# Kernel optimization log

Measured on AMD Instinct MI355X. Metric: run time of the kernel, lower is better.

Reference implementation:

```python
import jax, jax.numpy as jnp
import numpy as np

BN_EPS = 1e-5
SAMPLE_KEY = jax.random.key(42)


def setup_inputs() -> dict:
    key = jax.random.key(0)
    ks = jax.random.split(key, 12)
    B, W, E = 524288, 8, 4
    D = W * E  # 32, input dim of fc1

    def lin(k, fan_in, fan_out):
        k1, k2 = jax.random.split(k)
        bound = 1.0 / np.sqrt(fan_in)
        w = jax.random.uniform(k1, (fan_in, fan_out), jnp.float32, -bound, bound)
        b = jax.random.uniform(k2, (fan_out,), jnp.float32, -bound, bound)
        return w, b

    W1, b1 = lin(ks[0], D, 50)
    W2, b2 = lin(ks[1], 50, 30)
    W3, b3 = lin(ks[2], 30, 20)
    W4, b4 = lin(ks[3], 20, 15)
    W5, b5 = lin(ks[4], 15, W)
    # BatchNorm affine params (eval mode, running_mean=0, running_var=1)
    g1, be1 = jnp.ones((50,), jnp.float32), jnp.zeros((50,), jnp.float32)
    g2, be2 = jnp.ones((30,), jnp.float32), jnp.zeros((30,), jnp.float32)
    g3, be3 = jnp.ones((20,), jnp.float32), jnp.zeros((20,), jnp.float32)
    events = jax.random.normal(ks[5], (B, W, E), jnp.float32)
    return {"events": events,
            "W1": W1, "b1": b1, "g1": g1, "be1": be1,
            "W2": W2, "b2": b2, "g2": g2, "be2": be2,
            "W3": W3, "b3": b3, "g3": g3, "be3": be3,
            "W4": W4, "b4": b4, "W5": W5, "b5": b5}


def _bn_eval(x, g, b):
    # eval-mode BatchNorm1d with running_mean=0, running_var=1
    return x * (g / jnp.sqrt(1.0 + BN_EPS)) + b


def _probs(events, W1, b1, g1, be1, W2, b2, g2, be2, W3, b3, g3, be3, W4, b4, W5, b5):
    B = events.shape[0]
    x = events.reshape(B, -1)  # (B, window*event_size)
    h = jax.nn.relu(_bn_eval(x @ W1 + b1, g1, be1))
    h = jax.nn.relu(_bn_eval(h @ W2 + b2, g2, be2))
    h = jax.nn.relu(_bn_eval(h @ W3 + b3, g3, be3))
    h = jax.nn.relu(h @ W4 + b4)
    return jax.nn.sigmoid(h @ W5 + b5)  # (B, window_size)


def reference(events, W1, b1, g1, be1, W2, b2, g2, be2, W3, b3, g3, be3, W4, b4, W5, b5):
    p = _probs(events, W1, b1, g1, be1, W2, b2, g2, be2, W3, b3, g3, be3, W4, b4, W5, b5)
    # np.random.choice([0,1], p=[p, 1-p]) => P(choice=1) = 1 - p
    choice = jax.random.bernoulli(SAMPLE_KEY, 1.0 - p).astype(p.dtype)  # (B, W)
    chosen_events_np = 1.0 - choice
    flipped = jnp.abs(choice - p)            # prob of sampled outcome per element
    log_prob = jnp.log(jnp.prod(flipped, axis=1))  # (B,)
    return chosen_events_np, log_prob
```

## Files before the change

### kernel.cpp

```cpp
#include <hip/hip_runtime.h>
#include <math.h>

#define THREADS 256
#define P_MARGIN 1e-4f
#define FIXCAP 32

typedef float v2f __attribute__((ext_vector_type(2)));

__device__ __forceinline__ void tf2x32(unsigned x0, unsigned x1,
                                       unsigned &o0, unsigned &o1) {
  const unsigned k0 = 0u;
  const unsigned k1 = 42u;
  const unsigned k2 = 0x1BD11BDAu ^ k0 ^ k1;
  x0 += k0; x1 += k1;
#define TF_R(r) { x0 += x1; x1 = (x1 << (r)) | (x1 >> (32 - (r))); x1 ^= x0; }
  TF_R(13) TF_R(15) TF_R(26) TF_R(6)
  x0 += k1; x1 += k2 + 1u;
  TF_R(17) TF_R(29) TF_R(16) TF_R(24)
  x0 += k2; x1 += k0 + 2u;
  TF_R(13) TF_R(15) TF_R(26) TF_R(6)
  x0 += k0; x1 += k1 + 3u;
  TF_R(17) TF_R(29) TF_R(16) TF_R(24)
  x0 += k1; x1 += k2 + 4u;
  TF_R(13) TF_R(15) TF_R(26) TF_R(6)
  x0 += k2; x1 += k0 + 5u;
#undef TF_R
  o0 = x0; o1 = x1;
}

__global__ __launch_bounds__(THREADS, 2)
void wtf_kernel(const float* __restrict__ events,
                const float* __restrict__ W1, const float* __restrict__ b1,
                const float* __restrict__ g1, const float* __restrict__ be1,
                const float* __restrict__ W2, const float* __restrict__ b2,
                const float* __restrict__ g2, const float* __restrict__ be2,
                const float* __restrict__ W3, const float* __restrict__ b3,
                const float* __restrict__ g3, const float* __restrict__ be3,
                const float* __restrict__ W4, const float* __restrict__ b4,
                const float* __restrict__ W5, const float* __restrict__ b5,
                float* __restrict__ out_chosen,
                float* __restrict__ out_logp,
                int B) {
  __shared__ unsigned s_cnt;
  __shared__ unsigned s_rows[FIXCAP];
  __shared__ double sA[64];
  __shared__ double sB[64];
  __shared__ double sF[8];

  const int t = threadIdx.x;
  if (t == 0) s_cnt = 0;
  __syncthreads();

  const int b = blockIdx.x * THREADS + t;
  const bool active = (b < B);
  const float rden = (float)(1.0 / sqrt(1.0 + 1e-5));

  if (active) {
    float x[32];
    const float4* ev4 = reinterpret_cast<const float4*>(events) + (size_t)b * 8;
#pragma unroll
    for (int q = 0; q < 8; ++q) {
      float4 v = ev4[q];
      x[4 * q + 0] = v.x; x[4 * q + 1] = v.y; x[4 * q + 2] = v.z; x[4 * q + 3] = v.w;
    }

    v2f A[25];
#pragma unroll
    for (int j = 0; j < 25; ++j) A[j] = v2f{b1[2 * j], b1[2 * j + 1]};
#pragma unroll
    for (int k = 0; k < 32; ++k) {
      const v2f xk2 = {x[k], x[k]};
#pragma unroll
      for (int j = 0; j < 25; ++j) {
        v2f w = {W1[k * 50 + 2 * j], W1[k * 50 + 2 * j + 1]};
        A[j] = __builtin_elementwise_fma(xk2, w, A[j]);
      }
    }
    float a1[50];
#pragma unroll
    for (int j = 0; j < 25; ++j) {
      a1[2 * j + 0] = fmaxf(fmaf(A[j].x, g1[2 * j + 0] * rden, be1[2 * j + 0]), 0.f);
      a1[2 * j + 1] = fmaxf(fmaf(A[j].y, g1[2 * j + 1] * rden, be1[2 * j + 1]), 0.f);
    }

    v2f C[15];
#pragma unroll
    for (int j = 0; j < 15; ++j) C[j] = v2f{b2[2 * j], b2[2 * j + 1]};
#pragma unroll
    for (int k = 0; k < 50; ++k) {
      const v2f hk2 = {a1[k], a1[k]};
#pragma unroll
      for (int j = 0; j < 15; ++j) {
        v2f w = {W2[k * 30 + 2 * j], W2[k * 30 + 2 * j + 1]};
        C[j] = __builtin_elementwise_fma(hk2, w, C[j]);
      }
    }
    float a2[30];
#pragma unroll
    for (int j = 0; j < 15; ++j) {
      a2[2 * j + 0] = fmaxf(fmaf(C[j].x, g2[2 * j + 0] * rden, be2[2 * j + 0]), 0.f);
      a2[2 * j + 1] = fmaxf(fmaf(C[j].y, g2[2 * j + 1] * rden, be2[2 * j + 1]), 0.f);
    }

    v2f D[10];
#pragma unroll
    for (int j = 0; j < 10; ++j) D[j] = v2f{b3[2 * j], b3[2 * j + 1]};
#pragma unroll
    for (int k = 0; k < 30; ++k) {
      const v2f hk2 = {a2[k], a2[k]};
#pragma unroll
      for (int j = 0; j < 10; ++j) {
        v2f w = {W3[k * 20 + 2 * j], W3[k * 20 + 2 * j + 1]};
        D[j] = __builtin_elementwise_fma(hk2, w, D[j]);
      }
    }
    float a3[20];
#pragma unroll
    for (int j = 0; j < 10; ++j) {
      a3[2 * j + 0] = fmaxf(fmaf(D[j].x, g3[2 * j + 0] * rden, be3[2 * j + 0]), 0.f);
      a3[2 * j + 1] = fmaxf(fmaf(D[j].y, g3[2 * j + 1] * rden, be3[2 * j + 1]), 0.f);
    }

    v2f E[7];
    float e14 = b4[14];
#pragma unroll
    for (int j = 0; j < 7; ++j) E[j] = v2f{b4[2 * j], b4[2 * j + 1]};
#pragma unroll
    for (int k = 0; k < 20; ++k) {
      const float hk = a3[k];
      const v2f hk2 = {hk, hk};
#pragma unroll
      for (int j = 0; j < 7; ++j) {
        v2f w = {W4[k * 15 + 2 * j], W4[k * 15 + 2 * j + 1]};
        E[j] = __builtin_elementwise_fma(hk2, w, E[j]);
      }
      e14 = fmaf(hk, W4[k * 15 + 14], e14);
    }
    float a4[15];
#pragma unroll
    for (int j = 0; j < 7; ++j) {
      a4[2 * j + 0] = fmaxf(E[j].x, 0.f);
      a4[2 * j + 1] = fmaxf(E[j].y, 0.f);
    }
    a4[14] = fmaxf(e14, 0.f);

    v2f P[4];
#pragma unroll
    for (int j = 0; j < 4; ++j) P[j] = v2f{b5[2 * j], b5[2 * j + 1]};
#pragma unroll
    for (int k = 0; k < 15; ++k) {
      const v2f hk2 = {a4[k], a4[k]};
#pragma unroll
      for (int j = 0; j < 4; ++j) {
        v2f w = {W5[k * 8 + 2 * j], W5[k * 8 + 2 * j + 1]};
        P[j] = __builtin_elementwise_fma(hk2, w, P[j]);
      }
    }
    float p[8];
#pragma unroll
    for (int j = 0; j < 4; ++j) {
      p[2 * j + 0] = 1.f / (1.f + expf(-P[j].x));
      p[2 * j + 1] = 1.f / (1.f + expf(-P[j].y));
    }

    bool need = false;
    float prod = 1.f;
    float ch[8];
#pragma unroll
    for (int w = 0; w < 8; ++w) {
      unsigned j = 8u * (unsigned)b + (unsigned)w, o0, o1;
      tf2x32(0u, j, o0, o1);
      unsigned bits = o0 ^ o1;
      float u = __uint_as_float(0x3F800000u | (bits >> 9)) - 1.f;
      float thr = 1.f - p[w];
      bool choice = u < thr;
      need = need || (fabsf(u - thr) < P_MARGIN);
      ch[w] = choice ? 0.f : 1.f;
      prod *= choice ? thr : p[w];
    }
    if (need) {
      unsigned i = atomicAdd(&s_cnt, 1u);
      if (i < FIXCAP) s_rows[i] = (unsigned)b;
    }

    float4* oc = reinterpret_cast<float4*>(out_chosen) + (size_t)b * 2;
    oc[0] = make_float4(ch[0], ch[1], ch[2], ch[3]);
    oc[1] = make_float4(ch[4], ch[5], ch[6], ch[7]);
    out_logp[b] = logf(prod);
  }

  __syncthreads();
  unsigned cnt = s_cnt;
  if (cnt > FIXCAP) cnt = FIXCAP;
  if (cnt == 0) return;

  const double denom = sqrt(1.0 + 1e-5);
  for (unsigned r = 0; r < cnt; ++r) {
    const int rb = (int)s_rows[r];

    if (t < 32) sA[t] = (double)events[(size_t)rb * 32 + t];
    __syncthreads();

    double v = 0.0;
    if (t < 50) {
#pragma unroll
      for (int k = 0; k < 32; ++k) v = fma(sA[k], (double)W1[k * 50 + t], v);
      v += (double)b1[t];
      v = v * ((double)g1[t] / denom) + (double)be1[t];
      v = v > 0.0 ? v : 0.0;
    }
    __syncthreads();
    if (t < 50) sB[t] = v;
    __syncthreads();

    v = 0.0;
    if (t < 30) {
#pragma unroll
      for (int k = 0; k < 50; ++k) v = fma(sB[k], (double)W2[k * 30 + t], v);
      v += (double)b2[t];
      v = v * ((double)g2[t] / denom) + (double)be2[t];
      v = v > 0.0 ? v : 0.0;
    }
    __syncthreads();
    if (t < 30) sA[t] = v;
    __syncthreads();

    v = 0.0;
    if (t < 20) {
#pragma unroll
      for (int k = 0; k < 30; ++k) v = fma(sA[k], (double)W3[k * 20 + t], v);
      v += (double)b3[t];
      v = v * ((double)g3[t] / denom) + (double)be3[t];
      v = v > 0.0 ? v : 0.0;
    }
    __syncthreads();
    if (t < 20) sB[t] = v;
    __syncthreads();

    v = 0.0;
    if (t < 15) {
#pragma unroll
      for (int k = 0; k < 20; ++k) v = fma(sB[k], (double)W4[k * 15 + t], v);
      v += (double)b4[t];
      v = v > 0.0 ? v : 0.0;
    }
    __syncthreads();
    if (t < 15) sA[t] = v;
    __syncthreads();

    if (t < 8) {
      v = 0.0;
#pragma unroll
      for (int k = 0; k < 15; ++k) v = fma(sA[k], (double)W5[k * 8 + t], v);
      v += (double)b5[t];
      double p = 1.0 / (1.0 + exp(-v));
      unsigned j = 8u * (unsigned)rb + (unsigned)t, o0, o1;
      tf2x32(0u, j, o0, o1);
      unsigned bits = o0 ^ o1;
      float u = __uint_as_float(0x3F800000u | (bits >> 9)) - 1.f;
      double thr = 1.0 - p;
      bool choice = ((double)u < thr);
      out_chosen[(size_t)rb * 8 + t] = choice ? 0.f : 1.f;
      sF[t] = choice ? thr : p;
    }
    __syncthreads();
    if (t == 0) {
      double prod = 1.0;
      for (int w = 0; w < 8; ++w) prod *= sF[w];
      out_logp[rb] = (float)log(prod);
    }
    __syncthreads();
  }
}

extern "C" void kernel_launch(void* const* d_in, const int* in_sizes, int n_in,
                              void* d_out, int out_size, void* d_ws, size_t ws_size,
                              hipStream_t stream) {
  const float* events = (const float*)d_in[0];
  const float* W1  = (const float*)d_in[1];
  const float* b1  = (const float*)d_in[2];
  const float* g1  = (const float*)d_in[3];
  const float* be1 = (const float*)d_in[4];
  const float* W2  = (const float*)d_in[5];
  const float* b2  = (const float*)d_in[6];
  const float* g2  = (const float*)d_in[7];
  const float* be2 = (const float*)d_in[8];
  const float* W3  = (const float*)d_in[9];
  const float* b3  = (const float*)d_in[10];
  const float* g3  = (const float*)d_in[11];
  const float* be3 = (const float*)d_in[12];
  const float* W4  = (const float*)d_in[13];
  const float* b4  = (const float*)d_in[14];
  const float* W5  = (const float*)d_in[15];
  const float* b5  = (const float*)d_in[16];

  const int B = in_sizes[0] / 32;
  float* out = (float*)d_out;
  float* out_chosen = out;
  float* out_logp   = out + (size_t)B * 8;

  const int blocks = (B + THREADS - 1) / THREADS;
  hipLaunchKernelGGL(wtf_kernel, dim3(blocks), dim3(THREADS), 0, stream,
                     events, W1, b1, g1, be1, W2, b2, g2, be2,
                     W3, b3, g3, be3, W4, b4, W5, b5,
                     out_chosen, out_logp, B);
}
```

Measured before the change: 238.4 us.

## Process two rows per thread to reuse weight loads across rows

Each thread now computes the MLP for two batch rows, one block stride apart, so each weight pair loaded per layer feeds FMAs for both rows. This halves the number of weight loads per row and gives more independent FMA chains for instruction-level parallelism. The grid shrinks to match. The sigmoid exp and final log switch to the fast intrinsics __expf/__logf. The costs are higher register pressure, which may reduce occupancy, and an unguarded load of the second row's events when B is not a multiple of the rows per block.

```diff
diff --git a/kernel.cpp b/kernel.cpp
--- a/kernel.cpp
+++ b/kernel.cpp
@@ -2,6 +2,7 @@
 #include <math.h>
 
 #define THREADS 256
+#define ROWS 2
 #define P_MARGIN 1e-4f
 #define FIXCAP 32
 
@@ -51,142 +52,210 @@
   if (t == 0) s_cnt = 0;
   __syncthreads();
 
-  const int b = blockIdx.x * THREADS + t;
-  const bool active = (b < B);
+  const int row0 = blockIdx.x * (THREADS * ROWS) + t;
   const float rden = (float)(1.0 / sqrt(1.0 + 1e-5));
 
-  if (active) {
-    float x[32];
-    const float4* ev4 = reinterpret_cast<const float4*>(events) + (size_t)b * 8;
-#pragma unroll
-    for (int q = 0; q < 8; ++q) {
-      float4 v = ev4[q];
-      x[4 * q + 0] = v.x; x[4 * q + 1] = v.y; x[4 * q + 2] = v.z; x[4 * q + 3] = v.w;
-    }
-
-    v2f A[25];
-#pragma unroll
-    for (int j = 0; j < 25; ++j) A[j] = v2f{b1[2 * j], b1[2 * j + 1]};
+  bool act[ROWS];
+#pragma unroll
+  for (int r = 0; r < ROWS; ++r) act[r] = (row0 + r * THREADS) < B;
+
+  if (act[0]) {
+    float x[ROWS][32];
+#pragma unroll
+    for (int r = 0; r < ROWS; ++r) {
+      const float4* ev4 =
+          reinterpret_cast<const float4*>(events) + (size_t)(row0 + r * THREADS) * 8;
+#pragma unroll
+      for (int q = 0; q < 8; ++q) {
+        float4 v = ev4[q];
+        x[r][4 * q + 0] = v.x; x[r][4 * q + 1] = v.y;
+        x[r][4 * q + 2] = v.z; x[r][4 * q + 3] = v.w;
+      }
+    }
+
+    v2f A[ROWS][25];
+#pragma unroll
+    for (int j = 0; j < 25; ++j) {
+      const v2f bb = {b1[2 * j], b1[2 * j + 1]};
+#pragma unroll
+      for (int r = 0; r < ROWS; ++r) A[r][j] = bb;
+    }
 #pragma unroll
     for (int k = 0; k < 32; ++k) {
-      const v2f xk2 = {x[k], x[k]};
 #pragma unroll
       for (int j = 0; j < 25; ++j) {
-        v2f w = {W1[k * 50 + 2 * j], W1[k * 50 + 2 * j + 1]};
-        A[j] = __builtin_elementwise_fma(xk2, w, A[j]);
-      }
-    }
-    float a1[50];
+        const v2f w = {W1[k * 50 + 2 * j], W1[k * 50 + 2 * j + 1]};
+#pragma unroll
+        for (int r = 0; r < ROWS; ++r) {
+          const v2f xk2 = {x[r][k], x[r][k]};
+          A[r][j] = __builtin_elementwise_fma(xk2, w, A[r][j]);
+        }
+      }
+    }
+    float a1[ROWS][50];
 #pragma unroll
     for (int j = 0; j < 25; ++j) {
-      a1[2 * j + 0] = fmaxf(fmaf(A[j].x, g1[2 * j + 0] * rden, be1[2 * j + 0]), 0.f);
-      a1[2 * j + 1] = fmaxf(fmaf(A[j].y, g1[2 * j + 1] * rden, be1[2 * j + 1]), 0.f);
-    }
-
-    v2f C[15];
-#pragma unroll
-    for (int j = 0; j < 15; ++j) C[j] = v2f{b2[2 * j], b2[2 * j + 1]};
+      const float s0 = g1[2 * j + 0] * rden, s1 = g1[2 * j + 1] * rden;
+      const float o0 = be1[2 * j + 0],       o1 = be1[2 * j + 1];
+#pragma unroll
+      for (int r = 0; r < ROWS; ++r) {
+        a1[r][2 * j + 0] = fmaxf(fmaf(A[r][j].x, s0, o0), 0.f);
+        a1[r][2 * j + 1] = fmaxf(fmaf(A[r][j].y, s1, o1), 0.f);
+      }
+    }
+
+    v2f C[ROWS][15];
+#pragma unroll
+    for (int j = 0; j < 15; ++j) {
+      const v2f bb = {b2[2 * j], b2[2 * j + 1]};
+#pragma unroll
+      for (int r = 0; r < ROWS; ++r) C[r][j] = bb;
+    }
 #pragma unroll
     for (int k = 0; k < 50; ++k) {
-      const v2f hk2 = {a1[k], a1[k]};
 #pragma unroll
       for (int j = 0; j < 15; ++j) {
-        v2f w = {W2[k * 30 + 2 * j], W2[k * 30 + 2 * j + 1]};
-        C[j] = __builtin_elementwise_fma(hk2, w, C[j]);
-      }
-    }
-    float a2[30];
+        const v2f w = {W2[k * 30 + 2 * j], W2[k * 30 + 2 * j + 1]};
+#pragma unroll
+        for (int r = 0; r < ROWS; ++r) {
+          const v2f hk2 = {a1[r][k], a1[r][k]};
+          C[r][j] = __builtin_elementwise_fma(hk2, w, C[r][j]);
+        }
+      }
+    }
+    float a2[ROWS][30];
 #pragma unroll
     for (int j = 0; j < 15; ++j) {
-      a2[2 * j + 0] = fmaxf(fmaf(C[j].x, g2[2 * j + 0] * rden, be2[2 * j + 0]), 0.f);
-      a2[2 * j + 1] = fmaxf(fmaf(C[j].y, g2[2 * j + 1] * rden, be2[2 * j + 1]), 0.f);
-    }
-
-    v2f D[10];
-#pragma unroll
-    for (int j = 0; j < 10; ++j) D[j] = v2f{b3[2 * j], b3[2 * j + 1]};
+      const float s0 = g2[2 * j + 0] * rden, s1 = g2[2 * j + 1] * rden;
+      const float o0 = be2[2 * j + 0],       o1 = be2[2 * j + 1];
+#pragma unroll
+      for (int r = 0; r < ROWS; ++r) {
+        a2[r][2 * j + 0] = fmaxf(fmaf(C[r][j].x, s0, o0), 0.f);
+        a2[r][2 * j + 1] = fmaxf(fmaf(C[r][j].y, s1, o1), 0.f);
+      }
+    }
+
+    v2f D[ROWS][10];
+#pragma unroll
+    for (int j = 0; j < 10; ++j) {
+      const v2f bb = {b3[2 * j], b3[2 * j + 1]};
+#pragma unroll
+      for (int r = 0; r < ROWS; ++r) D[r][j] = bb;
+    }
 #pragma unroll
     for (int k = 0; k < 30; ++k) {
-      const v2f hk2 = {a2[k], a2[k]};
 #pragma unroll
       for (int j = 0; j < 10; ++j) {
-        v2f w = {W3[k * 20 + 2 * j], W3[k * 20 + 2 * j + 1]};
-        D[j] = __builtin_elementwise_fma(hk2, w, D[j]);
-      }
-    }
-    float a3[20];
+        const v2f w = {W3[k * 20 + 2 * j], W3[k * 20 + 2 * j + 1]};
+#pragma unroll
+        for (int r = 0; r < ROWS; ++r) {
+          const v2f hk2 = {a2[r][k], a2[r][k]};
+          D[r][j] = __builtin_elementwise_fma(hk2, w, D[r][j]);
+        }
+      }
+    }
+    float a3[ROWS][20];
 #pragma unroll
     for (int j = 0; j < 10; ++j) {
-      a3[2 * j + 0] = fmaxf(fmaf(D[j].x, g3[2 * j + 0] * rden, be3[2 * j + 0]), 0.f);
-      a3[2 * j + 1] = fmaxf(fmaf(D[j].y, g3[2 * j + 1] * rden, be3[2 * j + 1]), 0.f);
-    }
-
-    v2f E[7];
-    float e14 = b4[14];
-#pragma unroll
-    for (int j = 0; j < 7; ++j) E[j] = v2f{b4[2 * j], b4[2 * j + 1]};
+      const float s0 = g3[2 * j + 0] * rden, s1 = g3[2 * j + 1] * rden;
+      const float o0 = be3[2 * j + 0],       o1 = be3[2 * j + 1];
+#pragma unroll
+      for (int r = 0; r < ROWS; ++r) {
+        a3[r][2 * j + 0] = fmaxf(fmaf(D[r][j].x, s0, o0), 0.f);
+        a3[r][2 * j + 1] = fmaxf(fmaf(D[r][j].y, s1, o1), 0.f);
+      }
+    }
+
+    v2f E[ROWS][7];
+    float e14[ROWS];
+#pragma unroll
+    for (int j = 0; j < 7; ++j) {
+      const v2f bb = {b4[2 * j], b4[2 * j + 1]};
+#pragma unroll
+      for (int r = 0; r < ROWS; ++r) E[r][j] = bb;
+    }
+#pragma unroll
+    for (int r = 0; r < ROWS; ++r) e14[r] = b4[14];
 #pragma unroll
     for (int k = 0; k < 20; ++k) {
-      const float hk = a3[k];
-      const v2f hk2 = {hk, hk};
 #pragma unroll
       for (int j = 0; j < 7; ++j) {
-        v2f w = {W4[k * 15 + 2 * j], W4[k * 15 + 2 * j + 1]};
-        E[j] = __builtin_elementwise_fma(hk2, w, E[j]);
-      }
-      e14 = fmaf(hk, W4[k * 15 + 14], e14);
-    }
-    float a4[15];
-#pragma unroll
-    for (int j = 0; j < 7; ++j) {
-      a4[2 * j + 0] = fmaxf(E[j].x, 0.f);
-      a4[2 * j + 1] = fmaxf(E[j].y, 0.f);
-    }
-    a4[14] = fmaxf(e14, 0.f);
-
-    v2f P[4];
-#pragma unroll
-    for (int j = 0; j < 4; ++j) P[j] = v2f{b5[2 * j], b5[2 * j + 1]};
+        const v2f w = {W4[k * 15 + 2 * j], W4[k * 15 + 2 * j + 1]};
+#pragma unroll
+        for (int r = 0; r < ROWS; ++r) {
+          const v2f hk2 = {a3[r][k], a3[r][k]};
+          E[r][j] = __builtin_elementwise_fma(hk2, w, E[r][j]);
+        }
+      }
+      const float w14 = W4[k * 15 + 14];
+#pragma unroll
+      for (int r = 0; r < ROWS; ++r) e14[r] = fmaf(a3[r][k], w14, e14[r]);
+    }
+    float a4[ROWS][15];
+#pragma unroll
+    for (int r = 0; r < ROWS; ++r) {
+#pragma unroll
+      for (int j = 0; j < 7; ++j) {
+        a4[r][2 * j + 0] = fmaxf(E[r][j].x, 0.f);
+        a4[r][2 * j + 1] = fmaxf(E[r][j].y, 0.f);
+      }
+      a4[r][14] = fmaxf(e14[r], 0.f);
+    }
+
+    v2f P[ROWS][4];
+#pragma unroll
+    for (int j = 0; j < 4; ++j) {
+      const v2f bb = {b5[2 * j], b5[2 * j + 1]};
+#pragma unroll
+      for (int r = 0; r < ROWS; ++r) P[r][j] = bb;
+    }
 #pragma unroll
     for (int k = 0; k < 15; ++k) {
-      const v2f hk2 = {a4[k], a4[k]};
 #pragma unroll
       for (int j = 0; j < 4; ++j) {
-        v2f w = {W5[k * 8 + 2 * j], W5[k * 8 + 2 * j + 1]};
-        P[j] = __builtin_elementwise_fma(hk2, w, P[j]);
-      }
-    }
-    float p[8];
-#pragma unroll
-    for (int j = 0; j < 4; ++j) {
-      p[2 * j + 0] = 1.f / (1.f + expf(-P[j].x));
-      p[2 * j + 1] = 1.f / (1.f + expf(-P[j].y));
-    }
-
-    bool need = false;
-    float prod = 1.f;
-    float ch[8];
-#pragma unroll
-    for (int w = 0; w < 8; ++w) {
-      unsigned j = 8u * (unsigned)b + (unsigned)w, o0, o1;
-      tf2x32(0u, j, o0, o1);
-      unsigned bits = o0 ^ o1;
-      float u = __uint_as_float(0x3F800000u | (bits >> 9)) - 1.f;
-      float thr = 1.f - p[w];
-      bool choice = u < thr;
-      need = need || (fabsf(u - thr) < P_MARGIN);
-      ch[w] = choice ? 0.f : 1.f;
-      prod *= choice ? thr : p[w];
-    }
-    if (need) {
-      unsigned i = atomicAdd(&s_cnt, 1u);
-      if (i < FIXCAP) s_rows[i] = (unsigned)b;
-    }
-
-    float4* oc = reinterpret_cast<float4*>(out_chosen) + (size_t)b * 2;
-    oc[0] = make_float4(ch[0], ch[1], ch[2], ch[3]);
-    oc[1] = make_float4(ch[4], ch[5], ch[6], ch[7]);
-    out_logp[b] = logf(prod);
+        const v2f w = {W5[k * 8 + 2 * j], W5[k * 8 + 2 * j + 1]};
+#pragma unroll
+        for (int r = 0; r < ROWS; ++r) {
+          const v2f hk2 = {a4[r][k], a4[r][k]};
+          P[r][j] = __builtin_elementwise_fma(hk2, w, P[r][j]);
+        }
+      }
+    }
+
+#pragma unroll
+    for (int r = 0; r < ROWS; ++r) {
+      if (!act[r]) continue;
+      const int rb = row0 + r * THREADS;
+      float p[8];
+#pragma unroll
+      for (int j = 0; j < 4; ++j) {
+        p[2 * j + 0] = 1.f / (1.f + __expf(-P[r][j].x));
+        p[2 * j + 1] = 1.f / (1.f + __expf(-P[r][j].y));
+      }
+      bool need = false;
+      float prod = 1.f;
+      float ch[8];
+#pragma unroll
+      for (int w = 0; w < 8; ++w) {
+        unsigned j = 8u * (unsigned)rb + (unsigned)w, o0, o1;
+        tf2x32(0u, j, o0, o1);
+        unsigned bits = o0 ^ o1;
+        float u = __uint_as_float(0x3F800000u | (bits >> 9)) - 1.f;
+        float thr = 1.f - p[w];
+        bool choice = u < thr;
+        need = need || (fabsf(u - thr) < P_MARGIN);
+        ch[w] = choice ? 0.f : 1.f;
+        prod *= choice ? thr : p[w];
+      }
+      if (need) {
+        unsigned i = atomicAdd(&s_cnt, 1u);
+        if (i < FIXCAP) s_rows[i] = (unsigned)rb;
+      }
+      float4* oc = reinterpret_cast<float4*>(out_chosen) + (size_t)rb * 2;
+      oc[0] = make_float4(ch[0], ch[1], ch[2], ch[3]);
+      oc[1] = make_float4(ch[4], ch[5], ch[6], ch[7]);
+      out_logp[rb] = __logf(prod);
+    }
   }
 
   __syncthreads();
@@ -299,7 +368,8 @@
   float* out_chosen = out;
   float* out_logp   = out + (size_t)B * 8;
 
-  const int blocks = (B + THREADS - 1) / THREADS;
+  const int rows_per_block = THREADS * ROWS;
+  const int blocks = (B + rows_per_block - 1) / rows_per_block;
   hipLaunchKernelGGL(wtf_kernel, dim3(blocks), dim3(THREADS), 0, stream,
                      events, W1, b1, g1, be1, W2, b2, g2, be2,
                      W3, b3, g3, be3, W4, b4, W5, b5,
```

Result: slower. 487.2 us (+104.4%).

## Move MLP layers onto bf16x3 MFMA with LDS-staged weight fragments

Applied to the files above, without the earlier changes.

Replaces the per-thread scalar FMA MLP with wave-level 16x16x32 bf16 MFMA tiles. Precision is kept by splitting both activations and weights into hi/lo bf16 parts and issuing three MFMAs per tile. Weights are converted and laid out as MFMA fragments in LDS once per block, and each wave processes 8 tiles of 16 rows, passing activations between layers through padded LDS. The sampling epilogue is spread over 4 lanes per row with shuffle reductions, and the exact-fixup margin and capacity are widened to absorb the extra rounding error. This trades per-block staging cost, more LDS traffic and fast-math exp/log for much higher matrix throughput. Rows are no longer bounds-checked, so B must be a multiple of 512.

```diff
diff --git a/kernel.cpp b/kernel.cpp
--- a/kernel.cpp
+++ b/kernel.cpp
@@ -2,10 +2,35 @@
 #include <math.h>
 
 #define THREADS 256
-#define P_MARGIN 1e-4f
-#define FIXCAP 32
-
-typedef float v2f __attribute__((ext_vector_type(2)));
+#define TPW 8
+#define ROWS_PER_BLOCK 512
+#define P_MARGIN 2e-4f
+#define FIXCAP 64
+
+typedef float f32x4 __attribute__((ext_vector_type(4)));
+typedef short short8 __attribute__((ext_vector_type(8)));
+union Frag { unsigned u[4]; short8 s; };
+
+#define FR1 0
+#define FR2 2048
+#define FR3 4096
+#define FR4 5120
+#define FR5 5632
+#define VB1 6144
+#define VS1 6208
+#define VE1 6272
+#define VB2 6336
+#define VS2 6368
+#define VE2 6400
+#define VB3 6432
+#define VS3 6464
+#define VE3 6496
+#define VB4 6528
+#define VB5 6544
+#define ZEND 6560
+#define ACT 6560
+#define PT  10912
+#define WPOOL 11488
 
 __device__ __forceinline__ void tf2x32(unsigned x0, unsigned x1,
                                        unsigned &o0, unsigned &o1) {
@@ -28,6 +53,65 @@
   o0 = x0; o1 = x1;
 }
 
+__device__ __forceinline__ unsigned rtnb(float v) {
+  unsigned b = __float_as_uint(v);
+  return (b + 0x7FFFu + ((b >> 16) & 1u)) & 0xFFFF0000u;
+}
+
+__device__ __forceinline__ unsigned cvtpk(float a, float b) {
+  unsigned r;
+  asm("v_cvt_pk_bf16_f32 %0, %1, %2" : "=v"(r) : "v"(a), "v"(b));
+  return r;
+}
+
+__device__ __forceinline__ void pack8(const float f[8], short8 &H, short8 &L) {
+  Frag h, l;
+#pragma unroll
+  for (int d = 0; d < 4; ++d) {
+    unsigned hd = cvtpk(f[2 * d], f[2 * d + 1]);
+    h.u[d] = hd;
+    float r0 = f[2 * d]     - __uint_as_float(hd << 16);
+    float r1 = f[2 * d + 1] - __uint_as_float(hd & 0xFFFF0000u);
+    l.u[d] = cvtpk(r0, r1);
+  }
+  H = h.s; L = l.s;
+}
+
+__device__ __forceinline__ f32x4 mfma16(short8 a, short8 b, f32x4 c) {
+  return __builtin_amdgcn_mfma_f32_16x16x32_bf16(a, b, c, 0, 0, 0);
+}
+
+__device__ __forceinline__ short8 ldfrag(const float *sW, int dwoff) {
+  return *reinterpret_cast<const short8 *>(sW + dwoff);
+}
+
+template <int K, int N, int NT, int FB>
+__device__ __forceinline__ void stage_layer(const float *__restrict__ W,
+                                            float *sW, int t) {
+  for (int i = t; i < K * N; i += THREADS) {
+    int k = i / N, c = i - k * N;
+    float v = W[i];
+    unsigned hb = rtnb(v);
+    float lov = v - __uint_as_float(hb);
+    unsigned lb = rtnb(lov);
+    int kt = k >> 5, gg = (k >> 3) & 3, d = (k >> 1) & 3, par = k & 1;
+    int nt = c >> 4, lane = gg * 16 + (c & 15);
+    int combo = kt * NT + nt;
+    int dwhi = FB + (combo * 2 + 0) * 256 + lane * 4 + d;
+    unsigned short *hp = reinterpret_cast<unsigned short *>(sW);
+    hp[2 * dwhi + par] = (unsigned short)(hb >> 16);
+    hp[2 * (dwhi + 256) + par] = (unsigned short)(lb >> 16);
+  }
+}
+
+__device__ __forceinline__ void loadA(const float *actw, int kbase, int c,
+                                      int g, short8 &H, short8 &L) {
+  float f[8];
+#pragma unroll
+  for (int e = 0; e < 8; ++e) f[e] = actw[(kbase + g * 8 + e) * 17 + c];
+  pack8(f, H, L);
+}
+
 __global__ __launch_bounds__(THREADS, 2)
 void wtf_kernel(const float* __restrict__ events,
                 const float* __restrict__ W1, const float* __restrict__ b1,
@@ -41,6 +125,7 @@
                 float* __restrict__ out_chosen,
                 float* __restrict__ out_logp,
                 int B) {
+  __shared__ float sW[WPOOL];
   __shared__ unsigned s_cnt;
   __shared__ unsigned s_rows[FIXCAP];
   __shared__ double sA[64];
@@ -48,145 +133,172 @@
   __shared__ double sF[8];
 
   const int t = threadIdx.x;
+  const float rden = (float)(1.0 / sqrt(1.0 + 1e-5));
+
   if (t == 0) s_cnt = 0;
+  for (int i = t; i < ZEND; i += THREADS) sW[i] = 0.f;
   __syncthreads();
-
-  const int b = blockIdx.x * THREADS + t;
-  const bool active = (b < B);
-  const float rden = (float)(1.0 / sqrt(1.0 + 1e-5));
-
-  if (active) {
-    float x[32];
-    const float4* ev4 = reinterpret_cast<const float4*>(events) + (size_t)b * 8;
-#pragma unroll
-    for (int q = 0; q < 8; ++q) {
-      float4 v = ev4[q];
-      x[4 * q + 0] = v.x; x[4 * q + 1] = v.y; x[4 * q + 2] = v.z; x[4 * q + 3] = v.w;
-    }
-
-    v2f A[25];
-#pragma unroll
-    for (int j = 0; j < 25; ++j) A[j] = v2f{b1[2 * j], b1[2 * j + 1]};
-#pragma unroll
-    for (int k = 0; k < 32; ++k) {
-      const v2f xk2 = {x[k], x[k]};
-#pragma unroll
-      for (int j = 0; j < 25; ++j) {
-        v2f w = {W1[k * 50 + 2 * j], W1[k * 50 + 2 * j + 1]};
-        A[j] = __builtin_elementwise_fma(xk2, w, A[j]);
-      }
-    }
-    float a1[50];
-#pragma unroll
-    for (int j = 0; j < 25; ++j) {
-      a1[2 * j + 0] = fmaxf(fmaf(A[j].x, g1[2 * j + 0] * rden, be1[2 * j + 0]), 0.f);
-      a1[2 * j + 1] = fmaxf(fmaf(A[j].y, g1[2 * j + 1] * rden, be1[2 * j + 1]), 0.f);
-    }
-
-    v2f C[15];
-#pragma unroll
-    for (int j = 0; j < 15; ++j) C[j] = v2f{b2[2 * j], b2[2 * j + 1]};
-#pragma unroll
-    for (int k = 0; k < 50; ++k) {
-      const v2f hk2 = {a1[k], a1[k]};
-#pragma unroll
-      for (int j = 0; j < 15; ++j) {
-        v2f w = {W2[k * 30 + 2 * j], W2[k * 30 + 2 * j + 1]};
-        C[j] = __builtin_elementwise_fma(hk2, w, C[j]);
-      }
-    }
-    float a2[30];
-#pragma unroll
-    for (int j = 0; j < 15; ++j) {
-      a2[2 * j + 0] = fmaxf(fmaf(C[j].x, g2[2 * j + 0] * rden, be2[2 * j + 0]), 0.f);
-      a2[2 * j + 1] = fmaxf(fmaf(C[j].y, g2[2 * j + 1] * rden, be2[2 * j + 1]), 0.f);
-    }
-
-    v2f D[10];
-#pragma unroll
-    for (int j = 0; j < 10; ++j) D[j] = v2f{b3[2 * j], b3[2 * j + 1]};
-#pragma unroll
-    for (int k = 0; k < 30; ++k) {
-      const v2f hk2 = {a2[k], a2[k]};
-#pragma unroll
-      for (int j = 0; j < 10; ++j) {
-        v2f w = {W3[k * 20 + 2 * j], W3[k * 20 + 2 * j + 1]};
-        D[j] = __builtin_elementwise_fma(hk2, w, D[j]);
-      }
-    }
-    float a3[20];
-#pragma unroll
-    for (int j = 0; j < 10; ++j) {
-      a3[2 * j + 0] = fmaxf(fmaf(D[j].x, g3[2 * j + 0] * rden, be3[2 * j + 0]), 0.f);
-      a3[2 * j + 1] = fmaxf(fmaf(D[j].y, g3[2 * j + 1] * rden, be3[2 * j + 1]), 0.f);
-    }
-
-    v2f E[7];
-    float e14 = b4[14];
-#pragma unroll
-    for (int j = 0; j < 7; ++j) E[j] = v2f{b4[2 * j], b4[2 * j + 1]};
-#pragma unroll
-    for (int k = 0; k < 20; ++k) {
-      const float hk = a3[k];
-      const v2f hk2 = {hk, hk};
-#pragma unroll
-      for (int j = 0; j < 7; ++j) {
-        v2f w = {W4[k * 15 + 2 * j], W4[k * 15 + 2 * j + 1]};
-        E[j] = __builtin_elementwise_fma(hk2, w, E[j]);
-      }
-      e14 = fmaf(hk, W4[k * 15 + 14], e14);
-    }
-    float a4[15];
-#pragma unroll
-    for (int j = 0; j < 7; ++j) {
-      a4[2 * j + 0] = fmaxf(E[j].x, 0.f);
-      a4[2 * j + 1] = fmaxf(E[j].y, 0.f);
-    }
-    a4[14] = fmaxf(e14, 0.f);
-
-    v2f P[4];
-#pragma unroll
-    for (int j = 0; j < 4; ++j) P[j] = v2f{b5[2 * j], b5[2 * j + 1]};
-#pragma unroll
-    for (int k = 0; k < 15; ++k) {
-      const v2f hk2 = {a4[k], a4[k]};
-#pragma unroll
-      for (int j = 0; j < 4; ++j) {
-        v2f w = {W5[k * 8 + 2 * j], W5[k * 8 + 2 * j + 1]};
-        P[j] = __builtin_elementwise_fma(hk2, w, P[j]);
-      }
-    }
-    float p[8];
-#pragma unroll
-    for (int j = 0; j < 4; ++j) {
-      p[2 * j + 0] = 1.f / (1.f + expf(-P[j].x));
-      p[2 * j + 1] = 1.f / (1.f + expf(-P[j].y));
-    }
-
-    bool need = false;
-    float prod = 1.f;
-    float ch[8];
-#pragma unroll
-    for (int w = 0; w < 8; ++w) {
-      unsigned j = 8u * (unsigned)b + (unsigned)w, o0, o1;
-      tf2x32(0u, j, o0, o1);
-      unsigned bits = o0 ^ o1;
-      float u = __uint_as_float(0x3F800000u | (bits >> 9)) - 1.f;
-      float thr = 1.f - p[w];
-      bool choice = u < thr;
-      need = need || (fabsf(u - thr) < P_MARGIN);
-      ch[w] = choice ? 0.f : 1.f;
-      prod *= choice ? thr : p[w];
-    }
-    if (need) {
-      unsigned i = atomicAdd(&s_cnt, 1u);
-      if (i < FIXCAP) s_rows[i] = (unsigned)b;
-    }
-
-    float4* oc = reinterpret_cast<float4*>(out_chosen) + (size_t)b * 2;
-    oc[0] = make_float4(ch[0], ch[1], ch[2], ch[3]);
-    oc[1] = make_float4(ch[4], ch[5], ch[6], ch[7]);
-    out_logp[b] = logf(prod);
+  stage_layer<32, 50, 4, FR1>(W1, sW, t);
+  stage_layer<50, 30, 2, FR2>(W2, sW, t);
+  stage_layer<30, 20, 2, FR3>(W3, sW, t);
+  stage_layer<20, 15, 1, FR4>(W4, sW, t);
+  stage_layer<15, 8, 1, FR5>(W5, sW, t);
+  if (t < 50)                  { sW[VB1 + t] = b1[t]; sW[VS1 + t] = g1[t] * rden; sW[VE1 + t] = be1[t]; }
+  else if (t >= 64 && t < 94)  { int i = t - 64;  sW[VB2 + i] = b2[i]; sW[VS2 + i] = g2[i] * rden; sW[VE2 + i] = be2[i]; }
+  else if (t >= 128 && t < 148){ int i = t - 128; sW[VB3 + i] = b3[i]; sW[VS3 + i] = g3[i] * rden; sW[VE3 + i] = be3[i]; }
+  else if (t >= 192 && t < 207){ sW[VB4 + (t - 192)] = b4[t - 192]; }
+  else if (t >= 224 && t < 232){ sW[VB5 + (t - 224)] = b5[t - 224]; }
+  __syncthreads();
+
+  const int w = t >> 6, lane = t & 63;
+  const int c = lane & 15, g = lane >> 4;
+  float *actw = sW + ACT + w * 1088;
+  float *ptw  = sW + PT  + w * 144;
+
+#pragma unroll 1
+  for (int tt = 0; tt < TPW; ++tt) {
+    const int r0 = blockIdx.x * ROWS_PER_BLOCK + w * (TPW * 16) + tt * 16;
+
+    const float4 *xr = reinterpret_cast<const float4 *>(
+        events + (size_t)(r0 + c) * 32 + g * 8);
+    float4 xa = xr[0], xb = xr[1];
+    float xf[8] = {xa.x, xa.y, xa.z, xa.w, xb.x, xb.y, xb.z, xb.w};
+    short8 Xh, Xl; pack8(xf, Xh, Xl);
+
+    {
+      f32x4 acc[4];
+#pragma unroll
+      for (int nt = 0; nt < 4; ++nt) {
+        float bb = sW[VB1 + nt * 16 + c];
+        f32x4 ci = {bb, bb, bb, bb};
+        short8 bh = ldfrag(sW, FR1 + (nt * 2 + 0) * 256 + lane * 4);
+        short8 bl = ldfrag(sW, FR1 + (nt * 2 + 1) * 256 + lane * 4);
+        ci = mfma16(Xl, bh, ci);
+        ci = mfma16(Xh, bl, ci);
+        acc[nt] = mfma16(Xh, bh, ci);
+      }
+#pragma unroll
+      for (int nt = 0; nt < 4; ++nt) {
+        float sc = sW[VS1 + nt * 16 + c], of = sW[VE1 + nt * 16 + c];
+#pragma unroll
+        for (int r = 0; r < 4; ++r)
+          actw[(nt * 16 + c) * 17 + g * 4 + r] =
+              fmaxf(fmaf(acc[nt][r], sc, of), 0.f);
+      }
+    }
+
+    {
+      f32x4 acc[2];
+#pragma unroll
+      for (int nt = 0; nt < 2; ++nt) {
+        float bb = sW[VB2 + nt * 16 + c];
+        acc[nt] = f32x4{bb, bb, bb, bb};
+      }
+#pragma unroll
+      for (int kt = 0; kt < 2; ++kt) {
+        short8 Ah, Al; loadA(actw, kt * 32, c, g, Ah, Al);
+#pragma unroll
+        for (int nt = 0; nt < 2; ++nt) {
+          short8 bh = ldfrag(sW, FR2 + ((kt * 2 + nt) * 2 + 0) * 256 + lane * 4);
+          short8 bl = ldfrag(sW, FR2 + ((kt * 2 + nt) * 2 + 1) * 256 + lane * 4);
+          acc[nt] = mfma16(Al, bh, acc[nt]);
+          acc[nt] = mfma16(Ah, bl, acc[nt]);
+          acc[nt] = mfma16(Ah, bh, acc[nt]);
+        }
+      }
+#pragma unroll
+      for (int nt = 0; nt < 2; ++nt) {
+        float sc = sW[VS2 + nt * 16 + c], of = sW[VE2 + nt * 16 + c];
+#pragma unroll
+        for (int r = 0; r < 4; ++r)
+          actw[(nt * 16 + c) * 17 + g * 4 + r] =
+              fmaxf(fmaf(acc[nt][r], sc, of), 0.f);
+      }
+    }
+
+    {
+      f32x4 acc[2];
+#pragma unroll
+      for (int nt = 0; nt < 2; ++nt) {
+        float bb = sW[VB3 + nt * 16 + c];
+        acc[nt] = f32x4{bb, bb, bb, bb};
+      }
+      short8 Ah, Al; loadA(actw, 0, c, g, Ah, Al);
+#pragma unroll
+      for (int nt = 0; nt < 2; ++nt) {
+        short8 bh = ldfrag(sW, FR3 + (nt * 2 + 0) * 256 + lane * 4);
+        short8 bl = ldfrag(sW, FR3 + (nt * 2 + 1) * 256 + lane * 4);
+        acc[nt] = mfma16(Al, bh, acc[nt]);
+        acc[nt] = mfma16(Ah, bl, acc[nt]);
+        acc[nt] = mfma16(Ah, bh, acc[nt]);
+      }
+#pragma unroll
+      for (int nt = 0; nt < 2; ++nt) {
+        float sc = sW[VS3 + nt * 16 + c], of = sW[VE3 + nt * 16 + c];
+#pragma unroll
+        for (int r = 0; r < 4; ++r)
+          actw[(nt * 16 + c) * 17 + g * 4 + r] =
+              fmaxf(fmaf(acc[nt][r], sc, of), 0.f);
+      }
+    }
+
+    {
+      float bb = sW[VB4 + c];
+      f32x4 acc = {bb, bb, bb, bb};
+      short8 Ah, Al; loadA(actw, 0, c, g, Ah, Al);
+      short8 bh = ldfrag(sW, FR4 + 0 * 256 + lane * 4);
+      short8 bl = ldfrag(sW, FR4 + 1 * 256 + lane * 4);
+      acc = mfma16(Al, bh, acc);
+      acc = mfma16(Ah, bl, acc);
+      acc = mfma16(Ah, bh, acc);
+#pragma unroll
+      for (int r = 0; r < 4; ++r) {
+        actw[c * 17 + g * 4 + r] = fmaxf(acc[r], 0.f);
+        actw[(16 + c) * 17 + g * 4 + r] = 0.f;
+      }
+    }
+
+    {
+      float bb = sW[VB5 + c];
+      f32x4 acc = {bb, bb, bb, bb};
+      short8 Ah, Al; loadA(actw, 0, c, g, Ah, Al);
+      short8 bh = ldfrag(sW, FR5 + 0 * 256 + lane * 4);
+      short8 bl = ldfrag(sW, FR5 + 1 * 256 + lane * 4);
+      acc = mfma16(Al, bh, acc);
+      acc = mfma16(Ah, bl, acc);
+      acc = mfma16(Ah, bh, acc);
+      if (c < 8) {
+#pragma unroll
+        for (int r = 0; r < 4; ++r) ptw[(g * 4 + r) * 9 + c] = acc[r];
+      }
+    }
+
+    {
+      const int erow = lane >> 2, cp = lane & 3;
+      const int grow = r0 + erow;
+      float l0 = ptw[erow * 9 + 2 * cp];
+      float l1 = ptw[erow * 9 + 2 * cp + 1];
+      float p0 = 1.f / (1.f + __expf(-l0));
+      float p1 = 1.f / (1.f + __expf(-l1));
+      unsigned o0, o1, q0, q1;
+      tf2x32(0u, 8u * (unsigned)grow + 2u * cp,      o0, o1);
+      tf2x32(0u, 8u * (unsigned)grow + 2u * cp + 1u, q0, q1);
+      float u0 = __uint_as_float(0x3F800000u | ((o0 ^ o1) >> 9)) - 1.f;
+      float u1 = __uint_as_float(0x3F800000u | ((q0 ^ q1) >> 9)) - 1.f;
+      float th0 = 1.f - p0, th1 = 1.f - p1;
+      bool c0 = u0 < th0, c1 = u1 < th1;
+      bool need = (fabsf(u0 - th0) < P_MARGIN) || (fabsf(u1 - th1) < P_MARGIN);
+      float prod = (c0 ? th0 : p0) * (c1 ? th1 : p1);
+      prod *= __shfl_xor(prod, 1);
+      prod *= __shfl_xor(prod, 2);
+      float2 chv = make_float2(c0 ? 0.f : 1.f, c1 ? 0.f : 1.f);
+      *reinterpret_cast<float2 *>(out_chosen + (size_t)grow * 8 + 2 * cp) = chv;
+      if (cp == 0) out_logp[grow] = __logf(prod);
+      if (need) {
+        unsigned i = atomicAdd(&s_cnt, 1u);
+        if (i < FIXCAP) s_rows[i] = (unsigned)grow;
+      }
+    }
   }
 
   __syncthreads();
@@ -266,7 +378,7 @@
     __syncthreads();
     if (t == 0) {
       double prod = 1.0;
-      for (int w = 0; w < 8; ++w) prod *= sF[w];
+      for (int w2 = 0; w2 < 8; ++w2) prod *= sF[w2];
       out_logp[rb] = (float)log(prod);
     }
     __syncthreads();
@@ -299,7 +411,7 @@
   float* out_chosen = out;
   float* out_logp   = out + (size_t)B * 8;
 
-  const int blocks = (B + THREADS - 1) / THREADS;
+  const int blocks = (B + ROWS_PER_BLOCK - 1) / ROWS_PER_BLOCK;
   hipLaunchKernelGGL(wtf_kernel, dim3(blocks), dim3(THREADS), 0, stream,
                      events, W1, b1, g1, be1, W2, b2, g2, be2,
                      W3, b3, g3, be3, W4, b4, W5, b5,
```

Result: faster. 230.9 us (-3.2%).
